# Kernel optimization log

Measured on AMD Instinct MI355X. Metric: run time of the kernel, lower is better.

## Reference

```python
import jax, jax.numpy as jnp
import numpy as np

EPS_BN = 1e-5
NEG = -9e15


def _bn_train(x, g, b):
    # x: [B, C, N]; training-mode BatchNorm1d with batch stats (biased var)
    m = jnp.mean(x, axis=(0, 2), keepdims=True)
    v = jnp.mean((x - m) ** 2, axis=(0, 2), keepdims=True)
    return (x - m) * jax.lax.rsqrt(v + EPS_BN) * g[None, :, None] + b[None, :, None]


def _conv1x1(w, x, b=None):
    # w: [O, C], x: [B, C, N] -> [B, O, N]
    y = jnp.einsum('oc,bcn->bon', w, x)
    if b is not None:
        y = y + b[None, :, None]
    return y


def _sa_layer(x, maskb, qk_w, v_w, v_b, t_w, t_b, bn_g, bn_b):
    # x: [B, C, N], maskb: [B, N] bool
    q = jnp.einsum('hc,bcn->bhn', qk_w, x)          # shared q/k weights
    energy = jnp.einsum('bhn,bhm->bnm', q, q)        # [B, N, N]
    pair = maskb[:, :, None] & maskb[:, None, :]
    energy = jnp.where(pair, energy, NEG)
    attn = jax.nn.softmax(energy, axis=-1)
    attn = attn / (1e-9 + jnp.sum(attn, axis=1, keepdims=True))  # L1 renorm over dim=1
    x_v = _conv1x1(v_w, x, v_b)                      # [B, C, N]
    x_r = jnp.einsum('bcn,bnm->bcm', x_v, attn)      # bmm(x_v, attention)
    t = _conv1x1(t_w, x - x_r, t_b)
    x_r = jax.nn.relu(_bn_train(t, bn_g, bn_b))
    return x + x_r


def setup_inputs() -> dict:
    key = jax.random.key(0)
    ks = jax.random.split(key, 16)
    B, C, N = 16, 256, 2048
    H = C // 4
    s = 0.05
    inp = {
        'x': jax.random.normal(ks[0], (B, C, N), jnp.float32),
        'mask': jax.random.randint(ks[1], (B, N), 0, 2, jnp.int32),
        'conv1_w': jax.random.normal(ks[2], (C, C), jnp.float32) * s,
        'conv2_w': jax.random.normal(ks[3], (C, C), jnp.float32) * s,
        'bn1_g': jnp.ones((C,), jnp.float32),
        'bn1_b': jnp.zeros((C,), jnp.float32),
        'bn2_g': jnp.ones((C,), jnp.float32),
        'bn2_b': jnp.zeros((C,), jnp.float32),
        'sa_qk_w': jax.random.normal(ks[4], (4, H, C), jnp.float32) * s,
        'sa_v_w': jax.random.normal(ks[5], (4, C, C), jnp.float32) * s,
        'sa_v_b': jax.random.normal(ks[6], (4, C), jnp.float32) * s,
        'sa_t_w': jax.random.normal(ks[7], (4, C, C), jnp.float32) * s,
        'sa_t_b': jax.random.normal(ks[8], (4, C), jnp.float32) * s,
        'sa_bn_g': jnp.ones((4, C), jnp.float32),
        'sa_bn_b': jnp.zeros((4, C), jnp.float32),
    }
    return inp


def reference(x, mask, conv1_w, conv2_w, bn1_g, bn1_b, bn2_g, bn2_b,
              sa_qk_w, sa_v_w, sa_v_b, sa_t_w, sa_t_b, sa_bn_g, sa_bn_b):
    maskb = mask.astype(bool)
    x = jax.nn.relu(_bn_train(_conv1x1(conv1_w, x), bn1_g, bn1_b))
    x = jax.nn.relu(_bn_train(_conv1x1(conv2_w, x), bn2_g, bn2_b))
    outs = []
    for i in range(4):
        x = _sa_layer(x, maskb, sa_qk_w[i], sa_v_w[i], sa_v_b[i],
                      sa_t_w[i], sa_t_b[i], sa_bn_g[i], sa_bn_b[i])
        outs.append(x)
    return jnp.concatenate(outs, axis=1)  # [B, 4C, N]
```

## Files before the change

kernel.cpp:

```cpp
#include <hip/hip_runtime.h>
#include <math.h>

#define BB 16
#define CC 256
#define NN 2048
#define HH 64
#define NEGV (-9.0e15f)
#define ATTSC 4096.0f
#define ATTINV (1.0f/4096.0f)

typedef _Float16 f16x8 __attribute__((ext_vector_type(8)));
typedef float f32x4 __attribute__((ext_vector_type(4)));

__device__ __forceinline__ f32x4 mfma16(f16x8 a, f16x8 b, f32x4 c) {
  return __builtin_amdgcn_mfma_f32_16x16x32_f16(a, b, c, 0, 0, 0);
}
__device__ __forceinline__ unsigned short f2h(float f) {
  _Float16 h = (_Float16)f;
  return __builtin_bit_cast(unsigned short, h);
}
__device__ __forceinline__ float h2f(unsigned short u) {
  return (float)__builtin_bit_cast(_Float16, u);
}

__global__ __launch_bounds__(256)
void castw_kernel(const float* __restrict__ in, unsigned short* __restrict__ out, int n)
{
  const int i = blockIdx.x*256 + threadIdx.x;
  if (i < n) out[i] = f2h(in[i]);
}

__global__ __launch_bounds__(256)
void tcast_kernel(const float* __restrict__ src, long sstride,
                  unsigned short* __restrict__ dst)
{
  const int b = blockIdx.z, n0 = blockIdx.x*64, c0 = blockIdx.y*64;
  const int t = threadIdx.x;
  __shared__ float tile[64][66];
  const float* sb = src + (long)b*sstride;
  #pragma unroll
  for (int p = 0; p < 4; p++) {
    const int cr = (t>>4) + p*16;
    const int nq = (t&15)*4;
    const float4 v = *(const float4*)&sb[(long)(c0+cr)*NN + n0 + nq];
    tile[cr][nq+0] = v.x; tile[cr][nq+1] = v.y;
    tile[cr][nq+2] = v.z; tile[cr][nq+3] = v.w;
  }
  __syncthreads();
  unsigned short* db = dst + (long)b*NN*CC;
  #pragma unroll
  for (int p = 0; p < 4; p++) {
    const int nr = (t>>4) + p*16;
    const int cq = (t&15)*4;
    ushort4 o;
    o.x = f2h(tile[cq+0][nr]); o.y = f2h(tile[cq+1][nr]);
    o.z = f2h(tile[cq+2][nr]); o.w = f2h(tile[cq+3][nr]);
    *(ushort4*)&db[(long)(n0+nr)*CC + c0 + cq] = o;
  }
}

template<bool OHALF>
__global__ __launch_bounds__(256)
void gemm_xw_kernel(const unsigned short* __restrict__ A,
                    const unsigned short* __restrict__ W,
                    const float* __restrict__ bias,
                    void* __restrict__ out, int ocols)
{
  const int n0 = blockIdx.x*64, o0 = blockIdx.y*64, b = blockIdx.z;
  const int t = threadIdx.x;
  const int w = t >> 6, l = t & 63, lr = l & 15, lg = l >> 4;
  const int wr = w >> 1, wc = w & 1;
  __shared__ unsigned short Al[64][72];
  __shared__ unsigned short Bl[64][72];
  const unsigned short* Ab = A + ((long)b*NN + n0)*CC;
  const int srow = t >> 3, sg = t & 7;
  f32x4 acc[2][2];
  #pragma unroll
  for (int i = 0; i < 2; i++)
    #pragma unroll
    for (int j = 0; j < 2; j++) acc[i][j] = f32x4{0.f,0.f,0.f,0.f};

  for (int kt = 0; kt < 4; kt++) {
    const int k0 = kt*64;
    const uint4 a0 = *(const uint4*)&Ab[(long)srow*CC + k0 + sg*8];
    const uint4 a1 = *(const uint4*)&Ab[(long)(srow+32)*CC + k0 + sg*8];
    const uint4 w0 = *(const uint4*)&W[(long)(o0+srow)*CC + k0 + sg*8];
    const uint4 w1 = *(const uint4*)&W[(long)(o0+srow+32)*CC + k0 + sg*8];
    __syncthreads();
    *(uint4*)&Al[srow][sg*8] = a0;  *(uint4*)&Al[srow+32][sg*8] = a1;
    *(uint4*)&Bl[srow][sg*8] = w0;  *(uint4*)&Bl[srow+32][sg*8] = w1;
    __syncthreads();
    #pragma unroll
    for (int kf = 0; kf < 2; kf++) {
      f16x8 af0 = *(const f16x8*)&Al[wr*32 + lr]     [kf*32 + lg*8];
      f16x8 af1 = *(const f16x8*)&Al[wr*32 + 16 + lr][kf*32 + lg*8];
      f16x8 bf0 = *(const f16x8*)&Bl[wc*32 + lr]     [kf*32 + lg*8];
      f16x8 bf1 = *(const f16x8*)&Bl[wc*32 + 16 + lr][kf*32 + lg*8];
      acc[0][0] = mfma16(af0, bf0, acc[0][0]);
      acc[0][1] = mfma16(af0, bf1, acc[0][1]);
      acc[1][0] = mfma16(af1, bf0, acc[1][0]);
      acc[1][1] = mfma16(af1, bf1, acc[1][1]);
    }
  }
  #pragma unroll
  for (int j = 0; j < 2; j++) {
    const int oc = o0 + wc*32 + j*16 + lr;
    const float bo = bias ? bias[oc] : 0.f;
    #pragma unroll
    for (int i = 0; i < 2; i++) {
      const int nb = n0 + wr*32 + i*16 + lg*4;
      #pragma unroll
      for (int r = 0; r < 4; r++) {
        const float v = acc[i][j][r] + bo;
        const long idx = ((long)b*NN + nb + r)*ocols + oc;
        if (OHALF) ((unsigned short*)out)[idx] = f2h(v);
        else       ((float*)out)[idx] = v;
      }
    }
  }
}

__global__ __launch_bounds__(256)
void gemm_wx_kernel(const unsigned short* __restrict__ W,
                    const unsigned short* __restrict__ X,
                    const float* __restrict__ bias,
                    unsigned short* __restrict__ out)
{
  const int n0 = blockIdx.x*64, o0 = blockIdx.y*64, b = blockIdx.z;
  const int t = threadIdx.x;
  const int w = t >> 6, l = t & 63, lr = l & 15, lg = l >> 4;
  const int wr = w >> 1, wc = w & 1;
  __shared__ unsigned short Al[64][72];
  __shared__ unsigned short Bl[64][72];
  const unsigned short* Xb = X + ((long)b*NN + n0)*CC;
  const int srow = t >> 3, sg = t & 7;
  f32x4 acc[2][2];
  #pragma unroll
  for (int i = 0; i < 2; i++)
    #pragma unroll
    for (int j = 0; j < 2; j++) acc[i][j] = f32x4{0.f,0.f,0.f,0.f};

  for (int kt = 0; kt < 4; kt++) {
    const int k0 = kt*64;
    const uint4 w0 = *(const uint4*)&W[(long)(o0+srow)*CC + k0 + sg*8];
    const uint4 w1 = *(const uint4*)&W[(long)(o0+srow+32)*CC + k0 + sg*8];
    const uint4 x0 = *(const uint4*)&Xb[(long)srow*CC + k0 + sg*8];
    const uint4 x1 = *(const uint4*)&Xb[(long)(srow+32)*CC + k0 + sg*8];
    __syncthreads();
    *(uint4*)&Al[srow][sg*8] = w0;  *(uint4*)&Al[srow+32][sg*8] = w1;
    *(uint4*)&Bl[srow][sg*8] = x0;  *(uint4*)&Bl[srow+32][sg*8] = x1;
    __syncthreads();
    #pragma unroll
    for (int kf = 0; kf < 2; kf++) {
      f16x8 af0 = *(const f16x8*)&Al[wr*32 + lr]     [kf*32 + lg*8];
      f16x8 af1 = *(const f16x8*)&Al[wr*32 + 16 + lr][kf*32 + lg*8];
      f16x8 bf0 = *(const f16x8*)&Bl[wc*32 + lr]     [kf*32 + lg*8];
      f16x8 bf1 = *(const f16x8*)&Bl[wc*32 + 16 + lr][kf*32 + lg*8];
      acc[0][0] = mfma16(af0, bf0, acc[0][0]);
      acc[0][1] = mfma16(af0, bf1, acc[0][1]);
      acc[1][0] = mfma16(af1, bf0, acc[1][0]);
      acc[1][1] = mfma16(af1, bf1, acc[1][1]);
    }
  }
  #pragma unroll
  for (int j = 0; j < 2; j++) {
    const int nc = n0 + wc*32 + j*16 + lr;
    #pragma unroll
    for (int i = 0; i < 2; i++) {
      #pragma unroll
      for (int r = 0; r < 4; r++) {
        const int oc = o0 + wr*32 + i*16 + lg*4 + r;
        out[((long)b*CC + oc)*NN + nc] = f2h(acc[i][j][r] + bias[oc]);
      }
    }
  }
}

__global__ __launch_bounds__(256)
void rowstat_kernel(const unsigned short* __restrict__ qT, const int* __restrict__ mask,
                    float* __restrict__ rmax, float* __restrict__ rinv)
{
  const int b = blockIdx.y, n0 = blockIdx.x*64;
  const int t = threadIdx.x, w = t>>6, l = t&63, lr = l&15, lg = l>>4;
  __shared__ unsigned short qa[64][72];
  __shared__ unsigned short qb[64][72];
  __shared__ int ml[64];
  const int srow = t>>3, sg = t&7;
  const unsigned short* qbase = qT + (long)b*NN*HH;
  *(uint4*)&qa[srow][sg*8]    = *(const uint4*)&qbase[(long)(n0+srow)*HH + sg*8];
  *(uint4*)&qa[srow+32][sg*8] = *(const uint4*)&qbase[(long)(n0+srow+32)*HH + sg*8];
  int maskn[4];
  #pragma unroll
  for (int r = 0; r < 4; r++) maskn[r] = mask[(long)b*NN + n0 + w*16 + lg*4 + r];
  __syncthreads();
  f16x8 af0 = *(const f16x8*)&qa[w*16 + lr][lg*8];
  f16x8 af1 = *(const f16x8*)&qa[w*16 + lr][32 + lg*8];
  float mx[4], sm[4];
  #pragma unroll
  for (int r = 0; r < 4; r++) { mx[r] = -INFINITY; sm[r] = 0.f; }

  for (int m0 = 0; m0 < NN; m0 += 64) {
    __syncthreads();
    *(uint4*)&qb[srow][sg*8]    = *(const uint4*)&qbase[(long)(m0+srow)*HH + sg*8];
    *(uint4*)&qb[srow+32][sg*8] = *(const uint4*)&qbase[(long)(m0+srow+32)*HH + sg*8];
    if (t < 64) ml[t] = mask[(long)b*NN + m0 + t];
    __syncthreads();
    #pragma unroll
    for (int tm = 0; tm < 4; tm++) {
      f32x4 s = f32x4{0.f,0.f,0.f,0.f};
      s = mfma16(af0, *(const f16x8*)&qb[tm*16 + lr][lg*8],      s);
      s = mfma16(af1, *(const f16x8*)&qb[tm*16 + lr][32 + lg*8], s);
      const int cm = ml[tm*16 + lr];
      #pragma unroll
      for (int r = 0; r < 4; r++) {
        const float vm = (maskn[r] && cm) ? s[r] : NEGV;
        const float nm = fmaxf(mx[r], vm);
        sm[r] = sm[r]*__expf(mx[r]-nm) + __expf(vm-nm);
        mx[r] = nm;
      }
    }
  }
  #pragma unroll
  for (int off = 1; off < 16; off <<= 1) {
    #pragma unroll
    for (int r = 0; r < 4; r++) {
      const float om = __shfl_xor(mx[r], off, 64);
      const float os = __shfl_xor(sm[r], off, 64);
      const float nm = fmaxf(mx[r], om);
      sm[r] = sm[r]*__expf(mx[r]-nm) + os*__expf(om-nm);
      mx[r] = nm;
    }
  }
  if (lr == 0) {
    #pragma unroll
    for (int r = 0; r < 4; r++) {
      const long idx = (long)b*NN + n0 + w*16 + lg*4 + r;
      rmax[idx] = mx[r];
      rinv[idx] = 1.f/sm[r];
    }
  }
}

__global__ __launch_bounds__(256)
void yatt_kernel(const unsigned short* __restrict__ qT, const unsigned short* __restrict__ xv,
                 const int* __restrict__ mask, const float* __restrict__ rmax,
                 const float* __restrict__ rinv, float* __restrict__ xrT,
                 float* __restrict__ csum)
{
  const int b = blockIdx.y, m0 = blockIdx.x*64;
  const int t = threadIdx.x, w = t>>6, l = t&63, lr = l&15, lg = l>>4;
  __shared__ unsigned short qm[64][72];
  __shared__ unsigned short qn[64][72];
  __shared__ unsigned short at[64][72];
  __shared__ unsigned short xvl[256][72];
  __shared__ float rml[64], ril[64];
  __shared__ int mrl[64];
  const int srow = t>>3, sg = t&7;
  const unsigned short* qbase = qT + (long)b*NN*HH;
  const unsigned short* xvb = xv + (long)b*CC*NN;
  *(uint4*)&qm[srow][sg*8]    = *(const uint4*)&qbase[(long)(m0+srow)*HH + sg*8];
  *(uint4*)&qm[srow+32][sg*8] = *(const uint4*)&qbase[(long)(m0+srow+32)*HH + sg*8];
  int maskm[4];
  #pragma unroll
  for (int r = 0; r < 4; r++) maskm[r] = mask[(long)b*NN + m0 + w*16 + lg*4 + r];
  __syncthreads();
  f16x8 am0 = *(const f16x8*)&qm[w*16 + lr][lg*8];
  f16x8 am1 = *(const f16x8*)&qm[w*16 + lr][32 + lg*8];
  f32x4 acc[16];
  #pragma unroll
  for (int ct = 0; ct < 16; ct++) acc[ct] = f32x4{0.f,0.f,0.f,0.f};
  float cs[4] = {0.f, 0.f, 0.f, 0.f};

  for (int nc = 0; nc < NN; nc += 64) {
    __syncthreads();
    *(uint4*)&qn[srow][sg*8]    = *(const uint4*)&qbase[(long)(nc+srow)*HH + sg*8];
    *(uint4*)&qn[srow+32][sg*8] = *(const uint4*)&qbase[(long)(nc+srow+32)*HH + sg*8];
    if (t < 64) {
      rml[t] = rmax[(long)b*NN + nc + t];
      ril[t] = rinv[(long)b*NN + nc + t];
      mrl[t] = mask[(long)b*NN + nc + t];
    }
    #pragma unroll
    for (int i2 = 0; i2 < 8; i2++) {
      const int c = i2*32 + (t>>3);
      *(uint4*)&xvl[c][sg*8] = *(const uint4*)&xvb[(long)c*NN + nc + sg*8];
    }
    __syncthreads();
    #pragma unroll
    for (int tn = 0; tn < 4; tn++) {
      f32x4 s = f32x4{0.f,0.f,0.f,0.f};
      s = mfma16(am0, *(const f16x8*)&qn[tn*16 + lr][lg*8],      s);
      s = mfma16(am1, *(const f16x8*)&qn[tn*16 + lr][32 + lg*8], s);
      const int nn = tn*16 + lr;
      const int cm = mrl[nn];
      const float rm = rml[nn], ri = ril[nn];
      #pragma unroll
      for (int r = 0; r < 4; r++) {
        const float vm = (maskm[r] && cm) ? s[r] : NEGV;
        const float a_ = __expf(vm - rm) * ri;
        cs[r] += a_;
        at[w*16 + lg*4 + r][nn] = f2h(a_ * ATTSC);
      }
    }
    f16x8 aat0 = *(const f16x8*)&at[w*16 + lr][lg*8];
    f16x8 aat1 = *(const f16x8*)&at[w*16 + lr][32 + lg*8];
    #pragma unroll
    for (int ct = 0; ct < 16; ct++) {
      acc[ct] = mfma16(aat0, *(const f16x8*)&xvl[ct*16 + lr][lg*8],      acc[ct]);
      acc[ct] = mfma16(aat1, *(const f16x8*)&xvl[ct*16 + lr][32 + lg*8], acc[ct]);
    }
  }
  #pragma unroll
  for (int ct = 0; ct < 16; ct++) {
    #pragma unroll
    for (int r = 0; r < 4; r++)
      xrT[((long)b*NN + m0 + w*16 + lg*4 + r)*CC + ct*16 + lr] = acc[ct][r] * ATTINV;
  }
  #pragma unroll
  for (int off = 1; off < 16; off <<= 1) {
    #pragma unroll
    for (int r = 0; r < 4; r++) cs[r] += __shfl_xor(cs[r], off, 64);
  }
  if (lr == 0) {
    #pragma unroll
    for (int r = 0; r < 4; r++)
      csum[(long)b*NN + m0 + w*16 + lg*4 + r] = cs[r];
  }
}

__global__ __launch_bounds__(256)
void diff_kernel(const unsigned short* __restrict__ xT, const float* __restrict__ xrT,
                 const float* __restrict__ csumv, unsigned short* __restrict__ dT)
{
  const long i = (long)blockIdx.x*256 + threadIdx.x;
  const long base = i*8;
  const long row = base >> 8;
  const float inv = 1.f/(1e-9f + csumv[row]);
  const uint4 xu = *(const uint4*)&xT[base];
  const float4 y0 = *(const float4*)&xrT[base];
  const float4 y1 = *(const float4*)&xrT[base+4];
  const unsigned short* xs = (const unsigned short*)&xu;
  ushort4 o0, o1;
  o0.x = f2h(h2f(xs[0]) - y0.x*inv);
  o0.y = f2h(h2f(xs[1]) - y0.y*inv);
  o0.z = f2h(h2f(xs[2]) - y0.z*inv);
  o0.w = f2h(h2f(xs[3]) - y0.w*inv);
  o1.x = f2h(h2f(xs[4]) - y1.x*inv);
  o1.y = f2h(h2f(xs[5]) - y1.y*inv);
  o1.z = f2h(h2f(xs[6]) - y1.z*inv);
  o1.w = f2h(h2f(xs[7]) - y1.w*inv);
  *(ushort4*)&dT[base]   = o0;
  *(ushort4*)&dT[base+4] = o1;
}

__global__ __launch_bounds__(256)
void bnstatsA_kernel(const float* __restrict__ tT, float* __restrict__ part)
{
  const int k = blockIdx.x;
  const int c = threadIdx.x;
  float s = 0.f, sq = 0.f;
  const long r0 = (long)k*128;
  for (int r = 0; r < 128; r++) {
    const float v = tT[(r0 + r)*CC + c];
    s += v; sq += v*v;
  }
  part[(long)k*CC + c] = s;
  part[(long)(256 + k)*CC + c] = sq;
}

__global__ __launch_bounds__(1024)
void bnstatsB_kernel(const float* __restrict__ part,
                     float* __restrict__ mean, float* __restrict__ istd)
{
  const int t = threadIdx.x, c = t & 255, q = t >> 8;
  float s = 0.f, sq = 0.f;
  for (int k = q*64; k < q*64 + 64; k++) {
    s  += part[(long)k*CC + c];
    sq += part[(long)(256 + k)*CC + c];
  }
  __shared__ float ls[4][256], lq[4][256];
  ls[q][c] = s; lq[q][c] = sq;
  __syncthreads();
  if (q == 0) {
    s  = ls[0][c] + ls[1][c] + ls[2][c] + ls[3][c];
    sq = lq[0][c] + lq[1][c] + lq[2][c] + lq[3][c];
    const float mu = s / (float)(BB*NN);
    mean[c] = mu;
    istd[c] = rsqrtf(sq/(float)(BB*NN) - mu*mu + 1e-5f);
  }
}

__global__ __launch_bounds__(256)
void bnapplyA_kernel(const float* __restrict__ tT, const float* __restrict__ mean,
                     const float* __restrict__ istd, const float* __restrict__ g,
                     const float* __restrict__ bt, unsigned short* __restrict__ xTo)
{
  __shared__ float sc[CC], sh[CC];
  const int t = threadIdx.x;
  {
    const float is = istd[t], gg = g[t];
    sc[t] = is*gg; sh[t] = bt[t] - mean[t]*is*gg;
  }
  __syncthreads();
  const long i = (long)blockIdx.x*256 + t;
  const long base = i*8;
  const int c8 = (int)(base & 255);
  const float4 v0 = *(const float4*)&tT[base];
  const float4 v1 = *(const float4*)&tT[base+4];
  ushort4 o0, o1;
  o0.x = f2h(fmaxf(v0.x*sc[c8+0] + sh[c8+0], 0.f));
  o0.y = f2h(fmaxf(v0.y*sc[c8+1] + sh[c8+1], 0.f));
  o0.z = f2h(fmaxf(v0.z*sc[c8+2] + sh[c8+2], 0.f));
  o0.w = f2h(fmaxf(v0.w*sc[c8+3] + sh[c8+3], 0.f));
  o1.x = f2h(fmaxf(v1.x*sc[c8+4] + sh[c8+4], 0.f));
  o1.y = f2h(fmaxf(v1.y*sc[c8+5] + sh[c8+5], 0.f));
  o1.z = f2h(fmaxf(v1.z*sc[c8+6] + sh[c8+6], 0.f));
  o1.w = f2h(fmaxf(v1.w*sc[c8+7] + sh[c8+7], 0.f));
  *(ushort4*)&xTo[base]   = o0;
  *(ushort4*)&xTo[base+4] = o1;
}

__global__ __launch_bounds__(256)
void bnapplyT_kernel(const float* __restrict__ tT, const float* __restrict__ mean,
                     const float* __restrict__ istd, const float* __restrict__ g,
                     const float* __restrict__ bt, const float* __restrict__ resid,
                     long rstride, float* __restrict__ outp, long ostride)
{
  const int b = blockIdx.z, n0 = blockIdx.x*64, c0 = blockIdx.y*64;
  const int t = threadIdx.x;
  __shared__ float tile[64][66];
  const float* tb_ = tT + ((long)b*NN + n0)*CC;
  const int cq = (t&15)*4;
  float scv[4], shv[4];
  #pragma unroll
  for (int j = 0; j < 4; j++) {
    const int c = c0 + cq + j;
    const float is = istd[c], gg = g[c];
    scv[j] = is*gg; shv[j] = bt[c] - mean[c]*is*gg;
  }
  #pragma unroll
  for (int p = 0; p < 4; p++) {
    const int nr = (t>>4) + p*16;
    const float4 v = *(const float4*)&tb_[(long)nr*CC + c0 + cq];
    tile[cq+0][nr] = fmaxf(v.x*scv[0] + shv[0], 0.f);
    tile[cq+1][nr] = fmaxf(v.y*scv[1] + shv[1], 0.f);
    tile[cq+2][nr] = fmaxf(v.z*scv[2] + shv[2], 0.f);
    tile[cq+3][nr] = fmaxf(v.w*scv[3] + shv[3], 0.f);
  }
  __syncthreads();
  const int nq = (t&15)*4;
  #pragma unroll
  for (int p = 0; p < 4; p++) {
    const int cr = (t>>4) + p*16;
    float4 o;
    o.x = tile[cr][nq+0]; o.y = tile[cr][nq+1];
    o.z = tile[cr][nq+2]; o.w = tile[cr][nq+3];
    if (resid) {
      const float4 rv = *(const float4*)&resid[(long)b*rstride + (long)(c0+cr)*NN + n0 + nq];
      o.x += rv.x; o.y += rv.y; o.z += rv.z; o.w += rv.w;
    }
    *(float4*)&outp[(long)b*ostride + (long)(c0+cr)*NN + n0 + nq] = o;
  }
}

extern "C" void kernel_launch(void* const* d_in, const int* in_sizes, int n_in,
                              void* d_out, int out_size, void* d_ws, size_t ws_size,
                              hipStream_t stream)
{
  const float* x_in   = (const float*)d_in[0];
  const int*   mask   = (const int*)d_in[1];
  const float* conv1w = (const float*)d_in[2];
  const float* conv2w = (const float*)d_in[3];
  const float* bn1g   = (const float*)d_in[4];
  const float* bn1b   = (const float*)d_in[5];
  const float* bn2g   = (const float*)d_in[6];
  const float* bn2b   = (const float*)d_in[7];
  const float* qkw    = (const float*)d_in[8];
  const float* vw     = (const float*)d_in[9];
  const float* vb     = (const float*)d_in[10];
  const float* tw     = (const float*)d_in[11];
  const float* tb     = (const float*)d_in[12];
  const float* bng    = (const float*)d_in[13];
  const float* bnb    = (const float*)d_in[14];
  float* out = (float*)d_out;

  const long BCN = (long)BB*CC*NN;
  const long CN  = (long)CC*NN;
  char* p = (char*)d_ws;
  unsigned short* xTa = (unsigned short*)p; p += BCN*2;
  unsigned short* xTb = (unsigned short*)p; p += BCN*2;
  unsigned short* qTb = (unsigned short*)p; p += (long)BB*NN*HH*2;
  unsigned short* xvb = (unsigned short*)p; p += BCN*2;
  float* tT    = (float*)p; p += BCN*4;
  float* xbuf  = (float*)p; p += BCN*4;
  float* rmaxb = (float*)p; p += (long)BB*NN*4;
  float* rinvb = (float*)p; p += (long)BB*NN*4;
  float* csumb = (float*)p; p += (long)BB*NN*4;
  float* partb = (float*)p; p += 512L*CC*4;
  float* meanb = (float*)p; p += CC*4;
  float* istdb = (float*)p; p += CC*4;
  unsigned short* wc1 = (unsigned short*)p; p += (long)CC*CC*2;
  unsigned short* wc2 = (unsigned short*)p; p += (long)CC*CC*2;
  unsigned short* wqk = (unsigned short*)p; p += 4L*HH*CC*2;
  unsigned short* wv  = (unsigned short*)p; p += 4L*CC*CC*2;
  unsigned short* wt  = (unsigned short*)p; p += 4L*CC*CC*2;

  const dim3 gT(NN/64, CC/64, BB);
  const dim3 gQ(NN/64, 1, BB);
  const dim3 gRS(NN/64, BB);
  const dim3 blk(256);

  castw_kernel<<<dim3(256), blk, 0, stream>>>(conv1w, wc1, CC*CC);
  castw_kernel<<<dim3(256), blk, 0, stream>>>(conv2w, wc2, CC*CC);
  castw_kernel<<<dim3(256), blk, 0, stream>>>(qkw, wqk, 4*HH*CC);
  castw_kernel<<<dim3(1024), blk, 0, stream>>>(vw, wv, 4*CC*CC);
  castw_kernel<<<dim3(1024), blk, 0, stream>>>(tw, wt, 4*CC*CC);

  tcast_kernel<<<gT, blk, 0, stream>>>(x_in, CN, xTa);
  gemm_xw_kernel<false><<<gT, blk, 0, stream>>>(xTa, wc1, nullptr, tT, CC);
  bnstatsA_kernel<<<dim3(256), blk, 0, stream>>>(tT, partb);
  bnstatsB_kernel<<<dim3(1), dim3(1024), 0, stream>>>(partb, meanb, istdb);
  bnapplyA_kernel<<<dim3(4096), blk, 0, stream>>>(tT, meanb, istdb, bn1g, bn1b, xTb);
  gemm_xw_kernel<false><<<gT, blk, 0, stream>>>(xTb, wc2, nullptr, tT, CC);
  bnstatsA_kernel<<<dim3(256), blk, 0, stream>>>(tT, partb);
  bnstatsB_kernel<<<dim3(1), dim3(1024), 0, stream>>>(partb, meanb, istdb);
  bnapplyT_kernel<<<gT, blk, 0, stream>>>(tT, meanb, istdb, bn2g, bn2b,
                                          nullptr, 0, xbuf, CN);
  tcast_kernel<<<gT, blk, 0, stream>>>(xbuf, CN, xTa);

  unsigned short* cur = xTa;
  unsigned short* nxt = xTb;
  for (int i = 0; i < 4; i++) {
    gemm_xw_kernel<true><<<gQ, blk, 0, stream>>>(cur, wqk + (long)i*HH*CC, nullptr, qTb, HH);
    rowstat_kernel<<<gRS, blk, 0, stream>>>(qTb, mask, rmaxb, rinvb);
    gemm_wx_kernel<<<gT, blk, 0, stream>>>(wv + (long)i*CC*CC, cur, vb + (long)i*CC, xvb);
    yatt_kernel<<<gRS, blk, 0, stream>>>(qTb, xvb, mask, rmaxb, rinvb, tT, csumb);
    diff_kernel<<<dim3(4096), blk, 0, stream>>>(cur, tT, csumb, xvb);
    gemm_xw_kernel<false><<<gT, blk, 0, stream>>>(xvb, wt + (long)i*CC*CC, tb + (long)i*CC, tT, CC);
    bnstatsA_kernel<<<dim3(256), blk, 0, stream>>>(tT, partb);
    bnstatsB_kernel<<<dim3(1), dim3(1024), 0, stream>>>(partb, meanb, istdb);
    const float* resid = (i == 0) ? xbuf : (out + (long)(i-1)*CN);
    const long rstr = (i == 0) ? CN : 4*CN;
    bnapplyT_kernel<<<gT, blk, 0, stream>>>(tT, meanb, istdb,
                                            bng + (long)i*CC, bnb + (long)i*CC,
                                            resid, rstr, out + (long)i*CN, 4*CN);
    if (i < 3)
      tcast_kernel<<<gT, blk, 0, stream>>>(out + (long)i*CN, 4*CN, nxt);
    unsigned short* tmp = cur; cur = nxt; nxt = tmp;
  }

  (void)in_sizes; (void)n_in; (void)out_size; (void)ws_size;
}
```

Measured before the change: 954.8 us.

## Use fp16 intermediates, fuse BN-apply with transpose-cast, restructure attention kernels

Stores the conv/GEMM outputs and the attention result in fp16 instead of fp32, halving traffic for the BN-stats, BN-apply and diff kernels. Fuses the BN-apply with the transposed fp16 cast of the next layer input, removing a separate tcast pass. The attention kernels gain XOR-swizzled LDS, a block-index swizzle, batched online-softmax exponent updates, and a yatt restructure that loads the value tile straight into registers with a 4x4 MFMA tile per wave. The lower-precision intermediates may slightly change BN statistics and accuracy.

```diff
diff --git a/kernel.cpp b/kernel.cpp
--- a/kernel.cpp
+++ b/kernel.cpp
@@ -22,6 +22,12 @@
 __device__ __forceinline__ float h2f(unsigned short u) {
   return (float)__builtin_bit_cast(_Float16, u);
 }
+__device__ __forceinline__ unsigned short* sp(unsigned short* base, int row, int colh) {
+  return (unsigned short*)((char*)base + (row << 7) + (((colh << 1)) ^ ((row & 7) << 4)));
+}
+__device__ __forceinline__ const unsigned short* spc(const unsigned short* base, int row, int colh) {
+  return (const unsigned short*)((const char*)base + (row << 7) + (((colh << 1)) ^ ((row & 7) << 4)));
+}
 
 __global__ __launch_bounds__(256)
 void castw_kernel(const float* __restrict__ in, unsigned short* __restrict__ out, int n)
@@ -59,12 +65,11 @@
   }
 }
 
-template<bool OHALF>
 __global__ __launch_bounds__(256)
 void gemm_xw_kernel(const unsigned short* __restrict__ A,
                     const unsigned short* __restrict__ W,
                     const float* __restrict__ bias,
-                    void* __restrict__ out, int ocols)
+                    unsigned short* __restrict__ out, int ocols)
 {
   const int n0 = blockIdx.x*64, o0 = blockIdx.y*64, b = blockIdx.z;
   const int t = threadIdx.x;
@@ -110,12 +115,8 @@
     for (int i = 0; i < 2; i++) {
       const int nb = n0 + wr*32 + i*16 + lg*4;
       #pragma unroll
-      for (int r = 0; r < 4; r++) {
-        const float v = acc[i][j][r] + bo;
-        const long idx = ((long)b*NN + nb + r)*ocols + oc;
-        if (OHALF) ((unsigned short*)out)[idx] = f2h(v);
-        else       ((float*)out)[idx] = v;
-      }
+      for (int r = 0; r < 4; r++)
+        out[((long)b*NN + nb + r)*ocols + oc] = f2h(acc[i][j][r] + bo);
     }
   }
 }
@@ -180,44 +181,51 @@
 void rowstat_kernel(const unsigned short* __restrict__ qT, const int* __restrict__ mask,
                     float* __restrict__ rmax, float* __restrict__ rinv)
 {
-  const int b = blockIdx.y, n0 = blockIdx.x*64;
+  const int bid = blockIdx.x;
+  const int swz = (bid & 7)*64 + (bid >> 3);
+  const int b  = swz >> 5;
+  const int n0 = (swz & 31) * 64;
   const int t = threadIdx.x, w = t>>6, l = t&63, lr = l&15, lg = l>>4;
-  __shared__ unsigned short qa[64][72];
-  __shared__ unsigned short qb[64][72];
+  __shared__ unsigned short qs[64*64];
   __shared__ int ml[64];
   const int srow = t>>3, sg = t&7;
   const unsigned short* qbase = qT + (long)b*NN*HH;
-  *(uint4*)&qa[srow][sg*8]    = *(const uint4*)&qbase[(long)(n0+srow)*HH + sg*8];
-  *(uint4*)&qa[srow+32][sg*8] = *(const uint4*)&qbase[(long)(n0+srow+32)*HH + sg*8];
+  *(uint4*)sp(qs, srow,    sg*8) = *(const uint4*)&qbase[(long)(n0+srow)*HH + sg*8];
+  *(uint4*)sp(qs, srow+32, sg*8) = *(const uint4*)&qbase[(long)(n0+srow+32)*HH + sg*8];
   int maskn[4];
   #pragma unroll
   for (int r = 0; r < 4; r++) maskn[r] = mask[(long)b*NN + n0 + w*16 + lg*4 + r];
   __syncthreads();
-  f16x8 af0 = *(const f16x8*)&qa[w*16 + lr][lg*8];
-  f16x8 af1 = *(const f16x8*)&qa[w*16 + lr][32 + lg*8];
+  f16x8 af0 = *(const f16x8*)spc(qs, w*16 + lr, lg*8);
+  f16x8 af1 = *(const f16x8*)spc(qs, w*16 + lr, 32 + lg*8);
   float mx[4], sm[4];
   #pragma unroll
   for (int r = 0; r < 4; r++) { mx[r] = -INFINITY; sm[r] = 0.f; }
 
   for (int m0 = 0; m0 < NN; m0 += 64) {
     __syncthreads();
-    *(uint4*)&qb[srow][sg*8]    = *(const uint4*)&qbase[(long)(m0+srow)*HH + sg*8];
-    *(uint4*)&qb[srow+32][sg*8] = *(const uint4*)&qbase[(long)(m0+srow+32)*HH + sg*8];
+    *(uint4*)sp(qs, srow,    sg*8) = *(const uint4*)&qbase[(long)(m0+srow)*HH + sg*8];
+    *(uint4*)sp(qs, srow+32, sg*8) = *(const uint4*)&qbase[(long)(m0+srow+32)*HH + sg*8];
     if (t < 64) ml[t] = mask[(long)b*NN + m0 + t];
     __syncthreads();
+    float sv[4][4];
     #pragma unroll
     for (int tm = 0; tm < 4; tm++) {
       f32x4 s = f32x4{0.f,0.f,0.f,0.f};
-      s = mfma16(af0, *(const f16x8*)&qb[tm*16 + lr][lg*8],      s);
-      s = mfma16(af1, *(const f16x8*)&qb[tm*16 + lr][32 + lg*8], s);
+      s = mfma16(af0, *(const f16x8*)spc(qs, tm*16 + lr, lg*8),      s);
+      s = mfma16(af1, *(const f16x8*)spc(qs, tm*16 + lr, 32 + lg*8), s);
       const int cm = ml[tm*16 + lr];
       #pragma unroll
-      for (int r = 0; r < 4; r++) {
-        const float vm = (maskn[r] && cm) ? s[r] : NEGV;
-        const float nm = fmaxf(mx[r], vm);
-        sm[r] = sm[r]*__expf(mx[r]-nm) + __expf(vm-nm);
-        mx[r] = nm;
-      }
+      for (int r = 0; r < 4; r++) sv[tm][r] = (maskn[r] && cm) ? s[r] : NEGV;
+    }
+    #pragma unroll
+    for (int r = 0; r < 4; r++) {
+      const float tmx = fmaxf(fmaxf(sv[0][r], sv[1][r]), fmaxf(sv[2][r], sv[3][r]));
+      const float nm  = fmaxf(mx[r], tmx);
+      sm[r] = sm[r]*__expf(mx[r]-nm)
+            + __expf(sv[0][r]-nm) + __expf(sv[1][r]-nm)
+            + __expf(sv[2][r]-nm) + __expf(sv[3][r]-nm);
+      mx[r] = nm;
     }
   }
   #pragma unroll
@@ -244,53 +252,60 @@
 __global__ __launch_bounds__(256)
 void yatt_kernel(const unsigned short* __restrict__ qT, const unsigned short* __restrict__ xv,
                  const int* __restrict__ mask, const float* __restrict__ rmax,
-                 const float* __restrict__ rinv, float* __restrict__ xrT,
+                 const float* __restrict__ rinv, unsigned short* __restrict__ xrTh,
                  float* __restrict__ csum)
 {
-  const int b = blockIdx.y, m0 = blockIdx.x*64;
+  const int bid = blockIdx.x;
+  const int swz = (bid & 7)*64 + (bid >> 3);
+  const int b  = swz >> 5;
+  const int m0 = (swz & 31) * 64;
   const int t = threadIdx.x, w = t>>6, l = t&63, lr = l&15, lg = l>>4;
-  __shared__ unsigned short qm[64][72];
-  __shared__ unsigned short qn[64][72];
-  __shared__ unsigned short at[64][72];
-  __shared__ unsigned short xvl[256][72];
+  __shared__ unsigned short qn[64*64];
+  __shared__ unsigned short at[64*64];
   __shared__ float rml[64], ril[64];
   __shared__ int mrl[64];
   const int srow = t>>3, sg = t&7;
   const unsigned short* qbase = qT + (long)b*NN*HH;
   const unsigned short* xvb = xv + (long)b*CC*NN;
-  *(uint4*)&qm[srow][sg*8]    = *(const uint4*)&qbase[(long)(m0+srow)*HH + sg*8];
-  *(uint4*)&qm[srow+32][sg*8] = *(const uint4*)&qbase[(long)(m0+srow+32)*HH + sg*8];
+
+  *(uint4*)sp(at, srow,    sg*8) = *(const uint4*)&qbase[(long)(m0+srow)*HH + sg*8];
+  *(uint4*)sp(at, srow+32, sg*8) = *(const uint4*)&qbase[(long)(m0+srow+32)*HH + sg*8];
   int maskm[4];
   #pragma unroll
   for (int r = 0; r < 4; r++) maskm[r] = mask[(long)b*NN + m0 + w*16 + lg*4 + r];
   __syncthreads();
-  f16x8 am0 = *(const f16x8*)&qm[w*16 + lr][lg*8];
-  f16x8 am1 = *(const f16x8*)&qm[w*16 + lr][32 + lg*8];
-  f32x4 acc[16];
-  #pragma unroll
-  for (int ct = 0; ct < 16; ct++) acc[ct] = f32x4{0.f,0.f,0.f,0.f};
+  f16x8 am0 = *(const f16x8*)spc(at, w*16 + lr, lg*8);
+  f16x8 am1 = *(const f16x8*)spc(at, w*16 + lr, 32 + lg*8);
+
+  f32x4 acc[4][4];
+  #pragma unroll
+  for (int mi = 0; mi < 4; mi++)
+    #pragma unroll
+    for (int ci = 0; ci < 4; ci++) acc[mi][ci] = f32x4{0.f,0.f,0.f,0.f};
   float cs[4] = {0.f, 0.f, 0.f, 0.f};
 
   for (int nc = 0; nc < NN; nc += 64) {
     __syncthreads();
-    *(uint4*)&qn[srow][sg*8]    = *(const uint4*)&qbase[(long)(nc+srow)*HH + sg*8];
-    *(uint4*)&qn[srow+32][sg*8] = *(const uint4*)&qbase[(long)(nc+srow+32)*HH + sg*8];
+    *(uint4*)sp(qn, srow,    sg*8) = *(const uint4*)&qbase[(long)(nc+srow)*HH + sg*8];
+    *(uint4*)sp(qn, srow+32, sg*8) = *(const uint4*)&qbase[(long)(nc+srow+32)*HH + sg*8];
     if (t < 64) {
       rml[t] = rmax[(long)b*NN + nc + t];
       ril[t] = rinv[(long)b*NN + nc + t];
       mrl[t] = mask[(long)b*NN + nc + t];
     }
-    #pragma unroll
-    for (int i2 = 0; i2 < 8; i2++) {
-      const int c = i2*32 + (t>>3);
-      *(uint4*)&xvl[c][sg*8] = *(const uint4*)&xvb[(long)c*NN + nc + sg*8];
+    f16x8 xb0[4], xb1[4];
+    #pragma unroll
+    for (int ci = 0; ci < 4; ci++) {
+      const unsigned short* xp = &xvb[(long)(w*64 + ci*16 + lr)*NN + nc];
+      xb0[ci] = *(const f16x8*)(xp + lg*8);
+      xb1[ci] = *(const f16x8*)(xp + 32 + lg*8);
     }
     __syncthreads();
     #pragma unroll
     for (int tn = 0; tn < 4; tn++) {
       f32x4 s = f32x4{0.f,0.f,0.f,0.f};
-      s = mfma16(am0, *(const f16x8*)&qn[tn*16 + lr][lg*8],      s);
-      s = mfma16(am1, *(const f16x8*)&qn[tn*16 + lr][32 + lg*8], s);
+      s = mfma16(am0, *(const f16x8*)spc(qn, tn*16 + lr, lg*8),      s);
+      s = mfma16(am1, *(const f16x8*)spc(qn, tn*16 + lr, 32 + lg*8), s);
       const int nn = tn*16 + lr;
       const int cm = mrl[nn];
       const float rm = rml[nn], ri = ril[nn];
@@ -299,23 +314,36 @@
         const float vm = (maskm[r] && cm) ? s[r] : NEGV;
         const float a_ = __expf(vm - rm) * ri;
         cs[r] += a_;
-        at[w*16 + lg*4 + r][nn] = f2h(a_ * ATTSC);
+        *sp(at, w*16 + lg*4 + r, nn) = f2h(a_ * ATTSC);
       }
     }
-    f16x8 aat0 = *(const f16x8*)&at[w*16 + lr][lg*8];
-    f16x8 aat1 = *(const f16x8*)&at[w*16 + lr][32 + lg*8];
-    #pragma unroll
-    for (int ct = 0; ct < 16; ct++) {
-      acc[ct] = mfma16(aat0, *(const f16x8*)&xvl[ct*16 + lr][lg*8],      acc[ct]);
-      acc[ct] = mfma16(aat1, *(const f16x8*)&xvl[ct*16 + lr][32 + lg*8], acc[ct]);
-    }
-  }
-  #pragma unroll
-  for (int ct = 0; ct < 16; ct++) {
-    #pragma unroll
-    for (int r = 0; r < 4; r++)
-      xrT[((long)b*NN + m0 + w*16 + lg*4 + r)*CC + ct*16 + lr] = acc[ct][r] * ATTINV;
-  }
+    __syncthreads();
+    {
+      f16x8 aa[4];
+      #pragma unroll
+      for (int mi = 0; mi < 4; mi++) aa[mi] = *(const f16x8*)spc(at, mi*16 + lr, lg*8);
+      #pragma unroll
+      for (int ci = 0; ci < 4; ci++)
+        #pragma unroll
+        for (int mi = 0; mi < 4; mi++)
+          acc[mi][ci] = mfma16(aa[mi], xb0[ci], acc[mi][ci]);
+      #pragma unroll
+      for (int mi = 0; mi < 4; mi++) aa[mi] = *(const f16x8*)spc(at, mi*16 + lr, 32 + lg*8);
+      #pragma unroll
+      for (int ci = 0; ci < 4; ci++)
+        #pragma unroll
+        for (int mi = 0; mi < 4; mi++)
+          acc[mi][ci] = mfma16(aa[mi], xb1[ci], acc[mi][ci]);
+    }
+  }
+  #pragma unroll
+  for (int mi = 0; mi < 4; mi++)
+    #pragma unroll
+    for (int ci = 0; ci < 4; ci++)
+      #pragma unroll
+      for (int r = 0; r < 4; r++)
+        xrTh[((long)b*NN + m0 + mi*16 + lg*4 + r)*CC + w*64 + ci*16 + lr] =
+            f2h(acc[mi][ci][r] * ATTINV);
   #pragma unroll
   for (int off = 1; off < 16; off <<= 1) {
     #pragma unroll
@@ -329,7 +357,7 @@
 }
 
 __global__ __launch_bounds__(256)
-void diff_kernel(const unsigned short* __restrict__ xT, const float* __restrict__ xrT,
+void diff_kernel(const unsigned short* __restrict__ xT, const unsigned short* __restrict__ xrTh,
                  const float* __restrict__ csumv, unsigned short* __restrict__ dT)
 {
   const long i = (long)blockIdx.x*256 + threadIdx.x;
@@ -337,31 +365,25 @@
   const long row = base >> 8;
   const float inv = 1.f/(1e-9f + csumv[row]);
   const uint4 xu = *(const uint4*)&xT[base];
-  const float4 y0 = *(const float4*)&xrT[base];
-  const float4 y1 = *(const float4*)&xrT[base+4];
+  const uint4 yu = *(const uint4*)&xrTh[base];
   const unsigned short* xs = (const unsigned short*)&xu;
-  ushort4 o0, o1;
-  o0.x = f2h(h2f(xs[0]) - y0.x*inv);
-  o0.y = f2h(h2f(xs[1]) - y0.y*inv);
-  o0.z = f2h(h2f(xs[2]) - y0.z*inv);
-  o0.w = f2h(h2f(xs[3]) - y0.w*inv);
-  o1.x = f2h(h2f(xs[4]) - y1.x*inv);
-  o1.y = f2h(h2f(xs[5]) - y1.y*inv);
-  o1.z = f2h(h2f(xs[6]) - y1.z*inv);
-  o1.w = f2h(h2f(xs[7]) - y1.w*inv);
-  *(ushort4*)&dT[base]   = o0;
-  *(ushort4*)&dT[base+4] = o1;
-}
-
-__global__ __launch_bounds__(256)
-void bnstatsA_kernel(const float* __restrict__ tT, float* __restrict__ part)
+  const unsigned short* ys = (const unsigned short*)&yu;
+  uint4 ou;
+  unsigned short* os = (unsigned short*)&ou;
+  #pragma unroll
+  for (int j = 0; j < 8; j++) os[j] = f2h(h2f(xs[j]) - h2f(ys[j])*inv);
+  *(uint4*)&dT[base] = ou;
+}
+
+__global__ __launch_bounds__(256)
+void bnstatsA_kernel(const unsigned short* __restrict__ tTh, float* __restrict__ part)
 {
   const int k = blockIdx.x;
   const int c = threadIdx.x;
   float s = 0.f, sq = 0.f;
   const long r0 = (long)k*128;
   for (int r = 0; r < 128; r++) {
-    const float v = tT[(r0 + r)*CC + c];
+    const float v = h2f(tTh[(r0 + r)*CC + c]);
     s += v; sq += v*v;
   }
   part[(long)k*CC + c] = s;
@@ -391,7 +413,7 @@
 }
 
 __global__ __launch_bounds__(256)
-void bnapplyA_kernel(const float* __restrict__ tT, const float* __restrict__ mean,
+void bnapplyA_kernel(const unsigned short* __restrict__ tTh, const float* __restrict__ mean,
                      const float* __restrict__ istd, const float* __restrict__ g,
                      const float* __restrict__ bt, unsigned short* __restrict__ xTo)
 {
@@ -405,31 +427,27 @@
   const long i = (long)blockIdx.x*256 + t;
   const long base = i*8;
   const int c8 = (int)(base & 255);
-  const float4 v0 = *(const float4*)&tT[base];
-  const float4 v1 = *(const float4*)&tT[base+4];
-  ushort4 o0, o1;
-  o0.x = f2h(fmaxf(v0.x*sc[c8+0] + sh[c8+0], 0.f));
-  o0.y = f2h(fmaxf(v0.y*sc[c8+1] + sh[c8+1], 0.f));
-  o0.z = f2h(fmaxf(v0.z*sc[c8+2] + sh[c8+2], 0.f));
-  o0.w = f2h(fmaxf(v0.w*sc[c8+3] + sh[c8+3], 0.f));
-  o1.x = f2h(fmaxf(v1.x*sc[c8+4] + sh[c8+4], 0.f));
-  o1.y = f2h(fmaxf(v1.y*sc[c8+5] + sh[c8+5], 0.f));
-  o1.z = f2h(fmaxf(v1.z*sc[c8+6] + sh[c8+6], 0.f));
-  o1.w = f2h(fmaxf(v1.w*sc[c8+7] + sh[c8+7], 0.f));
-  *(ushort4*)&xTo[base]   = o0;
-  *(ushort4*)&xTo[base+4] = o1;
-}
-
-__global__ __launch_bounds__(256)
-void bnapplyT_kernel(const float* __restrict__ tT, const float* __restrict__ mean,
-                     const float* __restrict__ istd, const float* __restrict__ g,
-                     const float* __restrict__ bt, const float* __restrict__ resid,
-                     long rstride, float* __restrict__ outp, long ostride)
+  const uint4 v = *(const uint4*)&tTh[base];
+  const unsigned short* hs = (const unsigned short*)&v;
+  uint4 ou;
+  unsigned short* os = (unsigned short*)&ou;
+  #pragma unroll
+  for (int j = 0; j < 8; j++)
+    os[j] = f2h(fmaxf(h2f(hs[j])*sc[c8+j] + sh[c8+j], 0.f));
+  *(uint4*)&xTo[base] = ou;
+}
+
+__global__ __launch_bounds__(256)
+void bnfuse_kernel(const unsigned short* __restrict__ tTh, const float* __restrict__ mean,
+                   const float* __restrict__ istd, const float* __restrict__ g,
+                   const float* __restrict__ bt, const float* __restrict__ resid,
+                   long rstride, float* __restrict__ outp, long ostride,
+                   unsigned short* __restrict__ xtn)
 {
   const int b = blockIdx.z, n0 = blockIdx.x*64, c0 = blockIdx.y*64;
   const int t = threadIdx.x;
   __shared__ float tile[64][66];
-  const float* tb_ = tT + ((long)b*NN + n0)*CC;
+  const unsigned short* tb_ = tTh + ((long)b*NN + n0)*CC;
   const int cq = (t&15)*4;
   float scv[4], shv[4];
   #pragma unroll
@@ -441,11 +459,11 @@
   #pragma unroll
   for (int p = 0; p < 4; p++) {
     const int nr = (t>>4) + p*16;
-    const float4 v = *(const float4*)&tb_[(long)nr*CC + c0 + cq];
-    tile[cq+0][nr] = fmaxf(v.x*scv[0] + shv[0], 0.f);
-    tile[cq+1][nr] = fmaxf(v.y*scv[1] + shv[1], 0.f);
-    tile[cq+2][nr] = fmaxf(v.z*scv[2] + shv[2], 0.f);
-    tile[cq+3][nr] = fmaxf(v.w*scv[3] + shv[3], 0.f);
+    const ushort4 v = *(const ushort4*)&tb_[(long)nr*CC + c0 + cq];
+    tile[cq+0][nr] = fmaxf(h2f(v.x)*scv[0] + shv[0], 0.f);
+    tile[cq+1][nr] = fmaxf(h2f(v.y)*scv[1] + shv[1], 0.f);
+    tile[cq+2][nr] = fmaxf(h2f(v.z)*scv[2] + shv[2], 0.f);
+    tile[cq+3][nr] = fmaxf(h2f(v.w)*scv[3] + shv[3], 0.f);
   }
   __syncthreads();
   const int nq = (t&15)*4;
@@ -460,6 +478,19 @@
       o.x += rv.x; o.y += rv.y; o.z += rv.z; o.w += rv.w;
     }
     *(float4*)&outp[(long)b*ostride + (long)(c0+cr)*NN + n0 + nq] = o;
+    tile[cr][nq+0] = o.x; tile[cr][nq+1] = o.y;
+    tile[cr][nq+2] = o.z; tile[cr][nq+3] = o.w;
+  }
+  if (xtn) {
+    __syncthreads();
+    #pragma unroll
+    for (int p = 0; p < 4; p++) {
+      const int nr = (t>>4) + p*16;
+      ushort4 o;
+      o.x = f2h(tile[cq+0][nr]); o.y = f2h(tile[cq+1][nr]);
+      o.z = f2h(tile[cq+2][nr]); o.w = f2h(tile[cq+3][nr]);
+      *(ushort4*)&xtn[((long)b*NN + n0+nr)*CC + c0 + cq] = o;
+    }
   }
 }
 
@@ -487,11 +518,12 @@
   const long BCN = (long)BB*CC*NN;
   const long CN  = (long)CC*NN;
   char* p = (char*)d_ws;
-  unsigned short* xTa = (unsigned short*)p; p += BCN*2;
-  unsigned short* xTb = (unsigned short*)p; p += BCN*2;
-  unsigned short* qTb = (unsigned short*)p; p += (long)BB*NN*HH*2;
-  unsigned short* xvb = (unsigned short*)p; p += BCN*2;
-  float* tT    = (float*)p; p += BCN*4;
+  unsigned short* xTa  = (unsigned short*)p; p += BCN*2;
+  unsigned short* xTb  = (unsigned short*)p; p += BCN*2;
+  unsigned short* qTb  = (unsigned short*)p; p += (long)BB*NN*HH*2;
+  unsigned short* xvb  = (unsigned short*)p; p += BCN*2;
+  unsigned short* tTh  = (unsigned short*)p; p += BCN*2;
+  unsigned short* xrTh = (unsigned short*)p; p += BCN*2;
   float* xbuf  = (float*)p; p += BCN*4;
   float* rmaxb = (float*)p; p += (long)BB*NN*4;
   float* rinvb = (float*)p; p += (long)BB*NN*4;
@@ -507,7 +539,7 @@
 
   const dim3 gT(NN/64, CC/64, BB);
   const dim3 gQ(NN/64, 1, BB);
-  const dim3 gRS(NN/64, BB);
+  const dim3 gAtt(512);
   const dim3 blk(256);
 
   castw_kernel<<<dim3(256), blk, 0, stream>>>(conv1w, wc1, CC*CC);
@@ -517,35 +549,33 @@
   castw_kernel<<<dim3(1024), blk, 0, stream>>>(tw, wt, 4*CC*CC);
 
   tcast_kernel<<<gT, blk, 0, stream>>>(x_in, CN, xTa);
-  gemm_xw_kernel<false><<<gT, blk, 0, stream>>>(xTa, wc1, nullptr, tT, CC);
-  bnstatsA_kernel<<<dim3(256), blk, 0, stream>>>(tT, partb);
+  gemm_xw_kernel<<<gT, blk, 0, stream>>>(xTa, wc1, nullptr, tTh, CC);
+  bnstatsA_kernel<<<dim3(256), blk, 0, stream>>>(tTh, partb);
   bnstatsB_kernel<<<dim3(1), dim3(1024), 0, stream>>>(partb, meanb, istdb);
-  bnapplyA_kernel<<<dim3(4096), blk, 0, stream>>>(tT, meanb, istdb, bn1g, bn1b, xTb);
-  gemm_xw_kernel<false><<<gT, blk, 0, stream>>>(xTb, wc2, nullptr, tT, CC);
-  bnstatsA_kernel<<<dim3(256), blk, 0, stream>>>(tT, partb);
+  bnapplyA_kernel<<<dim3(4096), blk, 0, stream>>>(tTh, meanb, istdb, bn1g, bn1b, xTb);
+  gemm_xw_kernel<<<gT, blk, 0, stream>>>(xTb, wc2, nullptr, tTh, CC);
+  bnstatsA_kernel<<<dim3(256), blk, 0, stream>>>(tTh, partb);
   bnstatsB_kernel<<<dim3(1), dim3(1024), 0, stream>>>(partb, meanb, istdb);
-  bnapplyT_kernel<<<gT, blk, 0, stream>>>(tT, meanb, istdb, bn2g, bn2b,
-                                          nullptr, 0, xbuf, CN);
-  tcast_kernel<<<gT, blk, 0, stream>>>(xbuf, CN, xTa);
+  bnfuse_kernel<<<gT, blk, 0, stream>>>(tTh, meanb, istdb, bn2g, bn2b,
+                                        nullptr, 0, xbuf, CN, xTa);
 
   unsigned short* cur = xTa;
   unsigned short* nxt = xTb;
   for (int i = 0; i < 4; i++) {
-    gemm_xw_kernel<true><<<gQ, blk, 0, stream>>>(cur, wqk + (long)i*HH*CC, nullptr, qTb, HH);
-    rowstat_kernel<<<gRS, blk, 0, stream>>>(qTb, mask, rmaxb, rinvb);
+    gemm_xw_kernel<<<gQ, blk, 0, stream>>>(cur, wqk + (long)i*HH*CC, nullptr, qTb, HH);
+    rowstat_kernel<<<gAtt, blk, 0, stream>>>(qTb, mask, rmaxb, rinvb);
     gemm_wx_kernel<<<gT, blk, 0, stream>>>(wv + (long)i*CC*CC, cur, vb + (long)i*CC, xvb);
-    yatt_kernel<<<gRS, blk, 0, stream>>>(qTb, xvb, mask, rmaxb, rinvb, tT, csumb);
-    diff_kernel<<<dim3(4096), blk, 0, stream>>>(cur, tT, csumb, xvb);
-    gemm_xw_kernel<false><<<gT, blk, 0, stream>>>(xvb, wt + (long)i*CC*CC, tb + (long)i*CC, tT, CC);
-    bnstatsA_kernel<<<dim3(256), blk, 0, stream>>>(tT, partb);
+    yatt_kernel<<<gAtt, blk, 0, stream>>>(qTb, xvb, mask, rmaxb, rinvb, xrTh, csumb);
+    diff_kernel<<<dim3(4096), blk, 0, stream>>>(cur, xrTh, csumb, xvb);
+    gemm_xw_kernel<<<gT, blk, 0, stream>>>(xvb, wt + (long)i*CC*CC, tb + (long)i*CC, tTh, CC);
+    bnstatsA_kernel<<<dim3(256), blk, 0, stream>>>(tTh, partb);
     bnstatsB_kernel<<<dim3(1), dim3(1024), 0, stream>>>(partb, meanb, istdb);
     const float* resid = (i == 0) ? xbuf : (out + (long)(i-1)*CN);
     const long rstr = (i == 0) ? CN : 4*CN;
-    bnapplyT_kernel<<<gT, blk, 0, stream>>>(tT, meanb, istdb,
-                                            bng + (long)i*CC, bnb + (long)i*CC,
-                                            resid, rstr, out + (long)i*CN, 4*CN);
-    if (i < 3)
-      tcast_kernel<<<gT, blk, 0, stream>>>(out + (long)i*CN, 4*CN, nxt);
+    bnfuse_kernel<<<gT, blk, 0, stream>>>(tTh, meanb, istdb,
+                                          bng + (long)i*CC, bnb + (long)i*CC,
+                                          resid, rstr, out + (long)i*CN, 4*CN,
+                                          (i < 3) ? nxt : nullptr);
     unsigned short* tmp = cur; cur = nxt; nxt = tmp;
   }
 
```

Result: faster. 773.3 us (-19.0%).
